# Kernel tuning notes

Hardware: AMD Instinct MI355X
Metric: run time of the kernel (lower is better)

## Reference

```python
import jax, jax.numpy as jnp
import numpy as np

NPIX = 1024
NCHAN = 4
NVIS = 200000
CELL_SIZE = 0.005  # arcsec
ARCSEC = np.pi / (180.0 * 3600.0)
DL = CELL_SIZE * ARCSEC          # radians of sky per pixel
J = 6                            # KB kernel width (torchkbnufft numpoints default)
OSF = 2                          # grid oversampling (torchkbnufft default)
G = OSF * NPIX                   # oversampled grid size
BETA = 2.34 * J                  # KB shape parameter (kbwidth*numpoints)
UV_MAX_KLAMBDA = 8000.0


def _i0(x):
    # Abramowitz & Stegun 9.8.1/9.8.2 polynomial approximation of I0(x)
    ax = jnp.abs(x)
    ts = (ax / 3.75) ** 2
    small = 1.0 + ts * (3.5156229 + ts * (3.0899424 + ts * (1.2067492
            + ts * (0.2659732 + ts * (0.0360768 + ts * 0.0045813)))))
    t = 3.75 / jnp.maximum(ax, 3.75)
    big = (jnp.exp(ax) / jnp.sqrt(jnp.maximum(ax, 3.75))) * (0.39894228
          + t * (0.01328592 + t * (0.00225319 + t * (-0.00157565
          + t * (0.00916281 + t * (-0.02057706 + t * (0.02635537
          + t * (-0.01647633 + t * 0.00392377))))))))
    return jnp.where(ax <= 3.75, small, big)


def _kb_weights(dist):
    # Kaiser-Bessel interpolation kernel, support |u| <= J/2
    s = 1.0 - (2.0 * dist / J) ** 2
    w = _i0(BETA * jnp.sqrt(jnp.maximum(s, 0.0))) / J
    return jnp.where(s > 0.0, w, 0.0)


def _apodization():
    # 1 / (continuous FT of the KB kernel) sampled at centered image coords
    n = (jnp.arange(NPIX) - NPIX // 2).astype(jnp.float32) / G
    arg = BETA ** 2 - (np.pi * J * n) ** 2
    sq = jnp.sqrt(jnp.abs(arg))
    ft = jnp.where(arg > 0, jnp.sinh(sq) / sq, jnp.sinc(sq / np.pi))
    return 1.0 / ft  # [NPIX]


def _nufft(img, uu, vv):
    # --- apodize (de-apodization pre-compensation) and zero-pad ---
    apod = _apodization()
    c = img.astype(jnp.complex64) * (apod[:, None] * apod[None, :])
    grid = jnp.zeros((NCHAN, G, G), dtype=jnp.complex64)
    grid = grid.at[:, :NPIX, :NPIX].set(c)
    # center image on grid origin so phase center = image center
    grid = jnp.roll(grid, (-(NPIX // 2), -(NPIX // 2)), axis=(1, 2))
    F = jnp.fft.fft2(grid)  # [nchan, G, G] oversampled k-space

    # --- klambda -> radians/pixel -> fractional oversampled-grid index ---
    # radpix = klambda*1e3*2pi*DL ; t = radpix * G / (2pi)
    tx = uu * (1e3 * DL * G)
    ty = vv * (1e3 * DL * G)

    # --- KB interpolation over JxJ neighborhoods ---
    offs = (jnp.arange(J) - (J // 2 - 1)).astype(jnp.float32)
    iy_f = jnp.floor(ty)[:, None] + offs[None, :]   # [nvis, J]
    ix_f = jnp.floor(tx)[:, None] + offs[None, :]
    wy = _kb_weights(ty[:, None] - iy_f)            # [nvis, J]
    wx = _kb_weights(tx[:, None] - ix_f)
    iy = jnp.mod(iy_f.astype(jnp.int32), G)
    ix = jnp.mod(ix_f.astype(jnp.int32), G)

    patch = F[:, iy[:, :, None], ix[:, None, :]]    # [nchan, nvis, J, J]
    w2 = (wy[:, :, None] * wx[:, None, :]).astype(jnp.complex64)
    return jnp.einsum('ckab,kab->ck', patch, w2)    # [nchan, nvis]


def setup_inputs() -> dict:
    key = jax.random.key(0)
    k1, k2, k3 = jax.random.split(key, 3)
    img = jax.random.normal(k1, (NCHAN, NPIX, NPIX), dtype=jnp.float32)
    uu = (jax.random.uniform(k2, (NVIS,), dtype=jnp.float32) * 2.0 - 1.0) * UV_MAX_KLAMBDA
    vv = (jax.random.uniform(k3, (NVIS,), dtype=jnp.float32) * 2.0 - 1.0) * UV_MAX_KLAMBDA
    return {"img": img, "uu": uu, "vv": vv}


def reference(img, uu, vv):
    return _nufft(img, uu, vv)
```

## Files before the change

### kernel.cpp

```cpp
#include <hip/hip_runtime.h>
#include <hip/hip_fp16.h>
#include <math.h>

#define NPIXD 1024
#define GD    2048
#define NCHAND 4
#define NVISD 200000
#define KXROWS 408
#define YPACK  832
#define FINP   1024
#define IDX(i) ((i) + ((i) >> 4))
#define RSQ2   0.70710678118654752f

#define FH_SCALE   1048576.0f
#define FH_ISCALE  (1.0f / 1048576.0f)

static constexpr double PI_D = 3.14159265358979323846;
static constexpr float SCALE_F = (float)(1000.0 * 0.005 * PI_D / (180.0 * 3600.0) * 2048.0);
static constexpr float BETA_F  = (float)(2.34 * 6.0);

__global__ void setup_kernel(float* __restrict__ apod) {
    int i = blockIdx.x * 256 + threadIdx.x;
    if (i < NPIXD) {
        float n  = (float)(i - NPIXD / 2) / (float)GD;
        float t  = (float)(PI_D * 6.0) * n;
        float arg = BETA_F * BETA_F - t * t;
        float sq  = sqrtf(fabsf(arg));
        float ft  = (arg > 0.0f) ? (sinhf(sq) / sq)
                                 : ((sq == 0.0f) ? 1.0f : (sinf(sq) / sq));
        apod[i] = 1.0f / ft;
    }
}

__device__ __forceinline__ float2 cadd(float2 a, float2 b){ return make_float2(a.x+b.x, a.y+b.y); }
__device__ __forceinline__ float2 csub(float2 a, float2 b){ return make_float2(a.x-b.x, a.y-b.y); }
__device__ __forceinline__ float2 cmulf(float2 a, float2 b){ return make_float2(a.x*b.x - a.y*b.y, a.x*b.y + a.y*b.x); }
__device__ __forceinline__ float2 cnegi(float2 a){ return make_float2(a.y, -a.x); }

__device__ __forceinline__ float2 twf(float e) {
    float s, c;
    __sincosf(e * (float)(-PI_D / 1024.0), &s, &c);
    return make_float2(c, s);
}

__device__ __forceinline__ void dft8_sparse(float2 x0, float2 x1, float2 x6, float2 x7,
                                            float2 y[8]) {
    float2 u0 = cadd(x0,x6), u1 = csub(x0,x6), u2 = cadd(x1,x7), u3 = cnegi(csub(x1,x7));
    y[0]=cadd(u0,u2); y[2]=cadd(u1,u3); y[4]=csub(u0,u2); y[6]=csub(u1,u3);
    float2 o0 = x0;
    float2 o1 = make_float2(RSQ2*(x1.x + x1.y), RSQ2*(x1.y - x1.x));
    float2 o2 = make_float2(-x6.y, x6.x);
    float2 o3 = make_float2(RSQ2*(x7.x - x7.y), RSQ2*(x7.y + x7.x));
    float2 v0 = cadd(o0,o2), v1 = csub(o0,o2), v2 = cadd(o1,o3), v3 = cnegi(csub(o1,o3));
    y[1]=cadd(v0,v2); y[3]=cadd(v1,v3); y[5]=csub(v0,v2); y[7]=csub(v1,v3);
}

__device__ __forceinline__ void dft8_full(const float2 x[8], float2 y[8]) {
    float2 e0=cadd(x[0],x[4]), e1=cadd(x[1],x[5]), e2=cadd(x[2],x[6]), e3=cadd(x[3],x[7]);
    float2 o0=csub(x[0],x[4]), o1=csub(x[1],x[5]), o2=csub(x[2],x[6]), o3=csub(x[3],x[7]);
    o1 = make_float2(RSQ2*(o1.x + o1.y), RSQ2*(o1.y - o1.x));
    o2 = cnegi(o2);
    o3 = make_float2(RSQ2*(o3.y - o3.x), -RSQ2*(o3.x + o3.y));
    float2 u0=cadd(e0,e2), u1=csub(e0,e2), u2=cadd(e1,e3), u3=cnegi(csub(e1,e3));
    y[0]=cadd(u0,u2); y[2]=cadd(u1,u3); y[4]=csub(u0,u2); y[6]=csub(u1,u3);
    float2 v0=cadd(o0,o2), v1=csub(o0,o2), v2=cadd(o1,o3), v3=cnegi(csub(o1,o3));
    y[1]=cadd(v0,v2); y[3]=cadd(v1,v3); y[5]=csub(v0,v2); y[7]=csub(v1,v3);
}

__device__ __forceinline__ void stage0_ip(float2 x0, float2 x1, float2 x6, float2 x7,
                                          float2* __restrict__ buf) {
    int j = (int)threadIdx.x;
    float2 y[8];
    dft8_sparse(x0, x1, x6, x7, y);
    buf[IDX(8 * j)] = y[0];
    #pragma unroll
    for (int t = 1; t < 8; ++t)
        buf[IDX(8 * j + t)] = cmulf(twf((float)(t * j)), y[t]);
}

__device__ __forceinline__ void r8_ip(float2* __restrict__ buf, int m) {
    int j = (int)threadIdx.x;
    float2 x[8];
    #pragma unroll
    for (int k = 0; k < 8; ++k) x[k] = buf[IDX(j + 256 * k)];
    __syncthreads();
    float2 y[8];
    dft8_full(x, y);
    int pm = j & ~(m - 1);
    int base = 7 * pm + j;
    buf[IDX(base)] = y[0];
    #pragma unroll
    for (int t = 1; t < 8; ++t)
        buf[IDX(base + t * m)] = cmulf(twf((float)(t * pm)), y[t]);
}

__device__ __forceinline__ void r4_final_ip(float2* __restrict__ buf) {
    int j = (int)threadIdx.x;
    float2 v[8];
    #pragma unroll
    for (int h = 0; h < 2; ++h) {
        int jj = j + h * 256;
        v[h*4+0] = buf[IDX(jj)];
        v[h*4+1] = buf[IDX(jj + 512)];
        v[h*4+2] = buf[IDX(jj + 1024)];
        v[h*4+3] = buf[IDX(jj + 1536)];
    }
    __syncthreads();
    #pragma unroll
    for (int h = 0; h < 2; ++h) {
        int jj = j + h * 256;
        float2 a = v[h*4], b = v[h*4+1], cc = v[h*4+2], d = v[h*4+3];
        float2 u0 = cadd(a,cc), u1 = csub(a,cc), u2 = cadd(b,d), u3 = cnegi(csub(b,d));
        buf[IDX(jj)]        = cadd(u0,u2);
        buf[IDX(jj + 1536)] = csub(u1,u3);
    }
}

__global__ __launch_bounds__(256) void fft_rows_fused(const float* __restrict__ img,
                                                      const float* __restrict__ apod,
                                                      float2* __restrict__ Fin) {
    __shared__ float2 buf[2176];
    __shared__ float2 stg[KXROWS * 9];
    int j  = (int)threadIdx.x;
    int bx = (int)blockIdx.x;
    int c  = (int)blockIdx.y;
    int w  = (bx & 7) * 16 + (bx >> 3);
    int y0 = w * 4;
    float a0 = apod[j + 512], a1 = apod[j + 768], a6 = apod[j], a7 = apod[j + 256];
    float p1[4], p2[4];
    {
        const float* r1 = img + ((size_t)c * NPIXD + y0) * NPIXD;
        const float* r2 = img + ((size_t)c * NPIXD + y0 + 512) * NPIXD;
        p1[0]=r1[j+512]; p1[1]=r1[j+768]; p1[2]=r1[j]; p1[3]=r1[j+256];
        p2[0]=r2[j+512]; p2[1]=r2[j+768]; p2[2]=r2[j]; p2[3]=r2[j+256];
    }
    #pragma unroll
    for (int p = 0; p < 4; ++p) {
        int y1 = y0 + p;
        float ay1 = apod[y1], ay2 = apod[y1 + 512];
        float2 x0 = make_float2(p1[0]*a0*ay1, p2[0]*a0*ay2);
        float2 x1 = make_float2(p1[1]*a1*ay1, p2[1]*a1*ay2);
        float2 x6 = make_float2(p1[2]*a6*ay1, p2[2]*a6*ay2);
        float2 x7 = make_float2(p1[3]*a7*ay1, p2[3]*a7*ay2);
        if (p < 3) {
            const float* q1 = img + ((size_t)c * NPIXD + y1 + 1) * NPIXD;
            const float* q2 = img + ((size_t)c * NPIXD + y1 + 513) * NPIXD;
            p1[0]=q1[j+512]; p1[1]=q1[j+768]; p1[2]=q1[j]; p1[3]=q1[j+256];
            p2[0]=q2[j+512]; p2[1]=q2[j+768]; p2[2]=q2[j]; p2[3]=q2[j+256];
        }
        __syncthreads();
        stage0_ip(x0, x1, x6, x7, buf);
        __syncthreads();
        r8_ip(buf, 8);
        __syncthreads();
        r8_ip(buf, 64);
        __syncthreads();
        r4_final_ip(buf);
        __syncthreads();
        #pragma unroll
        for (int t = 0; t < 2; ++t) {
            int kx = j + t * 256;
            if (kx < KXROWS) {
                float2 Z  = buf[IDX(kx)];
                float2 Zm = buf[IDX((GD - kx) & (GD - 1))];
                stg[kx * 9 + p]     = make_float2(0.5f*(Z.x+Zm.x), 0.5f*(Z.y-Zm.y));
                stg[kx * 9 + 4 + p] = make_float2(0.5f*(Z.y+Zm.y), 0.5f*(Zm.x-Z.x));
            }
        }
    }
    __syncthreads();
    #pragma unroll
    for (int k = 0; k < 4; ++k) {
        int m = j + 256 * k;
        if (m < 2 * KXROWS) {
            int kx = m >> 1, h = m & 1;
            float2* dst = Fin + ((size_t)c * KXROWS + kx) * FINP + y0 + h * 512;
            const float2* s = &stg[kx * 9 + h * 4];
            dst[0] = s[0]; dst[1] = s[1]; dst[2] = s[2]; dst[3] = s[3];
        }
    }
}

__global__ __launch_bounds__(256) void fft_cols(const float2* __restrict__ Fin,
                                                __half* __restrict__ FhH,
                                                float* __restrict__ FhIm,
                                                int writeIm) {
    __shared__ float2 buf[2176];
    int j = (int)threadIdx.x;
    int kx = blockIdx.x, c = blockIdx.y;
    const float2* inr = Fin + ((size_t)c * KXROWS + kx) * FINP;
    float2 x0 = inr[j + 512];
    float2 x1 = inr[j + 768];
    float2 x6 = inr[j];
    float2 x7 = inr[j + 256];
    stage0_ip(x0, x1, x6, x7, buf);
    __syncthreads();
    r8_ip(buf, 8);
    __syncthreads();
    r8_ip(buf, 64);
    __syncthreads();
    r4_final_ip(buf);
    __syncthreads();
    __half* basep = FhH + ((size_t)kx * YPACK) * NCHAND + c;
    float*  imb   = FhIm + ((size_t)c * KXROWS + kx) * YPACK;
    for (int n = j; n < GD; n += 256) {
        int pos = -1;
        if (n < 416)         pos = n + 416;
        else if (n >= 1632)  pos = n - 1632;
        if (pos >= 0) {
            float2 z = buf[IDX(n)];
            basep[(size_t)pos * NCHAND] = __float2half_rn(z.x * FH_SCALE);
            if (writeIm) imb[pos] = z.y;
        }
    }
}

__device__ __forceinline__ float i0f(float x) {
    float ax = fabsf(x);
    if (ax <= 3.75f) {
        float ts = ax / 3.75f; ts *= ts;
        return 1.0f + ts * (3.5156229f + ts * (3.0899424f + ts * (1.2067492f +
                     ts * (0.2659732f + ts * (0.0360768f + ts * 0.0045813f)))));
    } else {
        float t = 3.75f / ax;
        return expf(ax) / sqrtf(ax) *
               (0.39894228f + t * (0.01328592f + t * (0.00225319f + t * (-0.00157565f +
                t * (0.00916281f + t * (-0.02057706f + t * (0.02635537f +
                t * (-0.01647633f + t * 0.00392377f))))))));
    }
}

__device__ __forceinline__ float kbwf(float dist) {
    float r = dist * (2.0f / 6.0f);
    float s = 1.0f - r * r;
    if (s <= 0.0f) return 0.0f;
    return i0f(BETA_F * sqrtf(s)) * (1.0f / 6.0f);
}

__global__ __launch_bounds__(256) void gather6(const float* __restrict__ uu,
                                               const float* __restrict__ vv,
                                               const float4* __restrict__ FhH4,
                                               const float* __restrict__ FhIm,
                                               float* __restrict__ out,
                                               int out_elems, int complexOut) {
    int tid = (int)threadIdx.x;
    int v = tid >> 1, r = tid & 1;
    int gv = blockIdx.x * 128 + v;
    if (gv >= NVISD) return;
    float tx = uu[gv] * SCALE_F;
    float ty = vv[gv] * SCALE_F;
    float fxf = floorf(tx), fyf = floorf(ty);
    int fxi = (int)fxf, fyi = (int)fyf;

    float wx[3]; int kxr[3]; int cjr[3];
    #pragma unroll
    for (int bb = 0; bb < 3; ++bb) {
        int b = r * 3 + bb, o = b - 2;
        wx[bb] = kbwf(tx - fxf - (float)o);
        int ix = (fxi + o) & (GD - 1);
        int cj = (ix > 1024) ? 1 : 0;
        int kx = cj ? (GD - ix) : ix;
        kxr[bb] = min(kx, KXROWS - 1);
        cjr[bb] = cj;
    }
    float wy[6];
    #pragma unroll
    for (int t = 0; t < 6; ++t) wy[t] = kbwf(ty - fyf - (float)(t - 2));

    int p0n = fyi + 414, p0c = 413 - fyi;
    p0n = min(max(p0n, 0), YPACK - 6);
    p0c = min(max(p0c, 0), YPACK - 6);
    int dn = p0n & 1, dc = p0c & 1;
    int f0n = (p0n - dn) >> 1, f0c = (p0c - dc) >> 1;
    float wn8[8], wc8[8];
    #pragma unroll
    for (int w = 0; w < 8; ++w) {
        int tn = w - dn; wn8[w] = (tn >= 0 && tn < 6) ? wy[tn] : 0.0f;
        int tc = w - dc; wc8[w] = (tc >= 0 && tc < 6) ? wy[5 - tc] : 0.0f;
    }

    float s0 = 0.0f, s1 = 0.0f, s2 = 0.0f, s3 = 0.0f;
    #pragma unroll
    for (int bb = 0; bb < 3; ++bb) {
        const float4* rp = FhH4 + (size_t)kxr[bb] * (YPACK / 2);
        bool cj = cjr[bb] != 0;
        int f0 = cj ? f0c : f0n;
        float wxb = wx[bb];
        #pragma unroll
        for (int q = 0; q < 4; ++q) {
            float4 Q = rp[f0 + q];
            float w0 = wxb * (cj ? wc8[2 * q]     : wn8[2 * q]);
            float w1 = wxb * (cj ? wc8[2 * q + 1] : wn8[2 * q + 1]);
            float2 fa = __half22float2(*reinterpret_cast<const __half2*>(&Q.x));
            float2 fb = __half22float2(*reinterpret_cast<const __half2*>(&Q.y));
            float2 fc = __half22float2(*reinterpret_cast<const __half2*>(&Q.z));
            float2 fd = __half22float2(*reinterpret_cast<const __half2*>(&Q.w));
            s0 = fmaf(w0, fa.x, fmaf(w1, fc.x, s0));
            s1 = fmaf(w0, fa.y, fmaf(w1, fc.y, s1));
            s2 = fmaf(w0, fb.x, fmaf(w1, fd.x, s2));
            s3 = fmaf(w0, fb.y, fmaf(w1, fd.y, s3));
        }
    }
    s0 += __shfl_xor(s0, 1);
    s1 += __shfl_xor(s1, 1);
    s2 += __shfl_xor(s2, 1);
    s3 += __shfl_xor(s3, 1);

    if (!complexOut) {
        if (r == 0 && (size_t)3 * NVISD + gv < (size_t)out_elems) {
            out[0 * NVISD + gv] = s0 * FH_ISCALE;
            out[1 * NVISD + gv] = s1 * FH_ISCALE;
            out[2 * NVISD + gv] = s2 * FH_ISCALE;
            out[3 * NVISD + gv] = s3 * FH_ISCALE;
        }
    } else {
        float sr[4] = {s0, s1, s2, s3};
        #pragma unroll
        for (int c = 0; c < NCHAND; ++c) {
            float sy = 0.0f;
            const float* baseI = FhIm + (size_t)c * KXROWS * YPACK;
            #pragma unroll
            for (int bb = 0; bb < 3; ++bb) {
                const float* rp = baseI + (size_t)kxr[bb] * YPACK;
                bool cj = cjr[bb] != 0;
                float wxb = wx[bb];
                #pragma unroll
                for (int a = 0; a < 6; ++a) {
                    int yv = fyi + (a - 2);
                    int pos = cj ? (416 - yv) : (yv + 416);
                    pos = min(max(pos, 0), YPACK - 1);
                    float w = wxb * wy[a];
                    sy = fmaf(cj ? -w : w, rp[pos], sy);
                }
            }
            sy += __shfl_xor(sy, 1);
            size_t oidx = (size_t)c * NVISD + gv;
            if (r == 0 && 2 * oidx + 1 < (size_t)out_elems) {
                out[2 * oidx] = sr[c] * FH_ISCALE;
                out[2 * oidx + 1] = sy;
            }
        }
    }
}

extern "C" void kernel_launch(void* const* d_in, const int* in_sizes, int n_in,
                              void* d_out, int out_size, void* d_ws, size_t ws_size,
                              hipStream_t stream) {
    (void)in_sizes; (void)n_in;
    const float* img = (const float*)d_in[0];
    const float* uu  = (const float*)d_in[1];
    const float* vv  = (const float*)d_in[2];

    const size_t apodBytes = 4096;
    const size_t finBytes  = (size_t)NCHAND * KXROWS * FINP * sizeof(float2);
    const size_t fhhBytes  = (size_t)KXROWS * YPACK * NCHAND * sizeof(__half);
    const size_t fhimBytes = (size_t)NCHAND * KXROWS * YPACK * sizeof(float);
    const size_t need = apodBytes + finBytes + fhhBytes + fhimBytes;

    char* ws = (char*)d_ws;
    float*  apod = (float*)ws;
    float2* Fin  = (float2*)(ws + apodBytes);
    __half* FhH  = (__half*)(ws + apodBytes + finBytes);
    float*  FhIm = (float*)(ws + apodBytes + finBytes + fhhBytes);

    if (ws_size < need) return;

    int complexOut = (out_size >= 2 * NCHAND * NVISD) ? 1 : 0;

    setup_kernel<<<dim3(4), dim3(256), 0, stream>>>(apod);
    fft_rows_fused<<<dim3(128, NCHAND), dim3(256), 0, stream>>>(img, apod, Fin);
    fft_cols<<<dim3(KXROWS, NCHAND), dim3(256), 0, stream>>>(Fin, FhH, FhIm, complexOut);
    gather6<<<dim3((NVISD + 127) / 128), dim3(256), 0, stream>>>(
        uu, vv, (const float4*)FhH, FhIm, (float*)d_out, out_size, complexOut);
}
```

Measured before the change: 54.96 us.

## Store row-FFT intermediate as fp16, inline apodization, ping-pong buffers, widen gather split

The intermediate row-FFT output is now stored as scaled half2 instead of float2, halving the traffic between the row and column FFT kernels. The apodization setup kernel is removed and its values are computed inline with __expf, which saves one launch. The row FFT uses two shared-memory ping-pong buffers, so one barrier per stage is dropped. The gather now uses four threads per visibility instead of two. The main risk is precision loss from fp16 storage of the intermediate, and the larger shared-memory footprint may reduce occupancy.

```diff
diff --git a/kernel.cpp b/kernel.cpp
--- a/kernel.cpp
+++ b/kernel.cpp
@@ -14,22 +14,21 @@
 
 #define FH_SCALE   1048576.0f
 #define FH_ISCALE  (1.0f / 1048576.0f)
+#define FIN_SCALE  4194304.0f
+#define FIN_TO_FH  0.25f
+#define FIN_TO_IM  (1.0f / 4194304.0f)
 
 static constexpr double PI_D = 3.14159265358979323846;
 static constexpr float SCALE_F = (float)(1000.0 * 0.005 * PI_D / (180.0 * 3600.0) * 2048.0);
 static constexpr float BETA_F  = (float)(2.34 * 6.0);
 
-__global__ void setup_kernel(float* __restrict__ apod) {
-    int i = blockIdx.x * 256 + threadIdx.x;
-    if (i < NPIXD) {
-        float n  = (float)(i - NPIXD / 2) / (float)GD;
-        float t  = (float)(PI_D * 6.0) * n;
-        float arg = BETA_F * BETA_F - t * t;
-        float sq  = sqrtf(fabsf(arg));
-        float ft  = (arg > 0.0f) ? (sinhf(sq) / sq)
-                                 : ((sq == 0.0f) ? 1.0f : (sinf(sq) / sq));
-        apod[i] = 1.0f / ft;
-    }
+__device__ __forceinline__ float apodf(int i) {
+    float n  = (float)(i - 512) * (1.0f / 2048.0f);
+    float t  = (float)(PI_D * 6.0) * n;
+    float arg = BETA_F * BETA_F - t * t;
+    float sq = sqrtf(arg);
+    float e  = __expf(sq);
+    return sq * 2.0f / (e - 1.0f / e);
 }
 
 __device__ __forceinline__ float2 cadd(float2 a, float2 b){ return make_float2(a.x+b.x, a.y+b.y); }
@@ -67,15 +66,43 @@
     y[1]=cadd(v0,v2); y[3]=cadd(v1,v3); y[5]=csub(v0,v2); y[7]=csub(v1,v3);
 }
 
-__device__ __forceinline__ void stage0_ip(float2 x0, float2 x1, float2 x6, float2 x7,
-                                          float2* __restrict__ buf) {
+__device__ __forceinline__ void stage0_st(float2 x0, float2 x1, float2 x6, float2 x7,
+                                          float2* __restrict__ dst) {
     int j = (int)threadIdx.x;
     float2 y[8];
     dft8_sparse(x0, x1, x6, x7, y);
-    buf[IDX(8 * j)] = y[0];
+    dst[IDX(8 * j)] = y[0];
     #pragma unroll
     for (int t = 1; t < 8; ++t)
-        buf[IDX(8 * j + t)] = cmulf(twf((float)(t * j)), y[t]);
+        dst[IDX(8 * j + t)] = cmulf(twf((float)(t * j)), y[t]);
+}
+
+__device__ __forceinline__ void r8_st(const float2* __restrict__ src, float2* __restrict__ dst,
+                                      int m) {
+    int j = (int)threadIdx.x;
+    float2 x[8], y[8];
+    #pragma unroll
+    for (int k = 0; k < 8; ++k) x[k] = src[IDX(j + 256 * k)];
+    dft8_full(x, y);
+    int pm = j & ~(m - 1);
+    int base = 7 * pm + j;
+    dst[IDX(base)] = y[0];
+    #pragma unroll
+    for (int t = 1; t < 8; ++t)
+        dst[IDX(base + t * m)] = cmulf(twf((float)(t * pm)), y[t]);
+}
+
+__device__ __forceinline__ void r4_final_st(const float2* __restrict__ src,
+                                            float2* __restrict__ dst) {
+    #pragma unroll
+    for (int h = 0; h < 2; ++h) {
+        int jj = (int)threadIdx.x + h * 256;
+        float2 a = src[IDX(jj)], b = src[IDX(jj + 512)];
+        float2 cc = src[IDX(jj + 1024)], d = src[IDX(jj + 1536)];
+        float2 u0 = cadd(a,cc), u1 = csub(a,cc), u2 = cadd(b,d), u3 = cnegi(csub(b,d));
+        dst[IDX(jj)]        = cadd(u0,u2);
+        dst[IDX(jj + 1536)] = csub(u1,u3);
+    }
 }
 
 __device__ __forceinline__ void r8_ip(float2* __restrict__ buf, int m) {
@@ -117,16 +144,19 @@
 }
 
 __global__ __launch_bounds__(256) void fft_rows_fused(const float* __restrict__ img,
-                                                      const float* __restrict__ apod,
-                                                      float2* __restrict__ Fin) {
-    __shared__ float2 buf[2176];
-    __shared__ float2 stg[KXROWS * 9];
+                                                      unsigned int* __restrict__ FinU) {
+    __shared__ float2 bufA[2176];
+    __shared__ float2 bufB[2176];
+    __shared__ unsigned int stg[KXROWS * 9];
     int j  = (int)threadIdx.x;
     int bx = (int)blockIdx.x;
     int c  = (int)blockIdx.y;
     int w  = (bx & 7) * 16 + (bx >> 3);
     int y0 = w * 4;
-    float a0 = apod[j + 512], a1 = apod[j + 768], a6 = apod[j], a7 = apod[j + 256];
+    float a0 = apodf(j + 512), a1 = apodf(j + 768), a6 = apodf(j), a7 = apodf(j + 256);
+    float ay[8];
+    #pragma unroll
+    for (int p = 0; p < 4; ++p) { ay[p] = apodf(y0 + p); ay[4 + p] = apodf(y0 + 512 + p); }
     float p1[4], p2[4];
     {
         const float* r1 = img + ((size_t)c * NPIXD + y0) * NPIXD;
@@ -136,35 +166,35 @@
     }
     #pragma unroll
     for (int p = 0; p < 4; ++p) {
-        int y1 = y0 + p;
-        float ay1 = apod[y1], ay2 = apod[y1 + 512];
+        float ay1 = ay[p], ay2 = ay[4 + p];
         float2 x0 = make_float2(p1[0]*a0*ay1, p2[0]*a0*ay2);
         float2 x1 = make_float2(p1[1]*a1*ay1, p2[1]*a1*ay2);
         float2 x6 = make_float2(p1[2]*a6*ay1, p2[2]*a6*ay2);
         float2 x7 = make_float2(p1[3]*a7*ay1, p2[3]*a7*ay2);
         if (p < 3) {
-            const float* q1 = img + ((size_t)c * NPIXD + y1 + 1) * NPIXD;
-            const float* q2 = img + ((size_t)c * NPIXD + y1 + 513) * NPIXD;
+            const float* q1 = img + ((size_t)c * NPIXD + y0 + p + 1) * NPIXD;
+            const float* q2 = img + ((size_t)c * NPIXD + y0 + p + 513) * NPIXD;
             p1[0]=q1[j+512]; p1[1]=q1[j+768]; p1[2]=q1[j]; p1[3]=q1[j+256];
             p2[0]=q2[j+512]; p2[1]=q2[j+768]; p2[2]=q2[j]; p2[3]=q2[j+256];
         }
+        stage0_st(x0, x1, x6, x7, bufA);
         __syncthreads();
-        stage0_ip(x0, x1, x6, x7, buf);
+        r8_st(bufA, bufB, 8);
         __syncthreads();
-        r8_ip(buf, 8);
+        r8_st(bufB, bufA, 64);
         __syncthreads();
-        r8_ip(buf, 64);
-        __syncthreads();
-        r4_final_ip(buf);
+        r4_final_st(bufA, bufB);
         __syncthreads();
         #pragma unroll
         for (int t = 0; t < 2; ++t) {
             int kx = j + t * 256;
             if (kx < KXROWS) {
-                float2 Z  = buf[IDX(kx)];
-                float2 Zm = buf[IDX((GD - kx) & (GD - 1))];
-                stg[kx * 9 + p]     = make_float2(0.5f*(Z.x+Zm.x), 0.5f*(Z.y-Zm.y));
-                stg[kx * 9 + 4 + p] = make_float2(0.5f*(Z.y+Zm.y), 0.5f*(Zm.x-Z.x));
+                float2 Z  = bufB[IDX(kx)];
+                float2 Zm = bufB[IDX((GD - kx) & (GD - 1))];
+                __half2 h1 = __floats2half2_rn(0.5f*(Z.x+Zm.x)*FIN_SCALE, 0.5f*(Z.y-Zm.y)*FIN_SCALE);
+                __half2 h2 = __floats2half2_rn(0.5f*(Z.y+Zm.y)*FIN_SCALE, 0.5f*(Zm.x-Z.x)*FIN_SCALE);
+                stg[kx * 9 + p]     = *reinterpret_cast<unsigned int*>(&h1);
+                stg[kx * 9 + 4 + p] = *reinterpret_cast<unsigned int*>(&h2);
             }
         }
     }
@@ -174,26 +204,27 @@
         int m = j + 256 * k;
         if (m < 2 * KXROWS) {
             int kx = m >> 1, h = m & 1;
-            float2* dst = Fin + ((size_t)c * KXROWS + kx) * FINP + y0 + h * 512;
-            const float2* s = &stg[kx * 9 + h * 4];
-            dst[0] = s[0]; dst[1] = s[1]; dst[2] = s[2]; dst[3] = s[3];
-        }
-    }
-}
-
-__global__ __launch_bounds__(256) void fft_cols(const float2* __restrict__ Fin,
+            unsigned int* dst = FinU + ((size_t)c * KXROWS + kx) * FINP + y0 + h * 512;
+            const unsigned int* s = &stg[kx * 9 + h * 4];
+            *reinterpret_cast<uint4*>(dst) = make_uint4(s[0], s[1], s[2], s[3]);
+        }
+    }
+}
+
+__global__ __launch_bounds__(256) void fft_cols(const unsigned int* __restrict__ FinU,
                                                 __half* __restrict__ FhH,
                                                 float* __restrict__ FhIm,
                                                 int writeIm) {
     __shared__ float2 buf[2176];
     int j = (int)threadIdx.x;
     int kx = blockIdx.x, c = blockIdx.y;
-    const float2* inr = Fin + ((size_t)c * KXROWS + kx) * FINP;
-    float2 x0 = inr[j + 512];
-    float2 x1 = inr[j + 768];
-    float2 x6 = inr[j];
-    float2 x7 = inr[j + 256];
-    stage0_ip(x0, x1, x6, x7, buf);
+    const unsigned int* inr = FinU + ((size_t)c * KXROWS + kx) * FINP;
+    unsigned int u0 = inr[j + 512], u1 = inr[j + 768], u6 = inr[j], u7 = inr[j + 256];
+    float2 x0 = __half22float2(*reinterpret_cast<__half2*>(&u0));
+    float2 x1 = __half22float2(*reinterpret_cast<__half2*>(&u1));
+    float2 x6 = __half22float2(*reinterpret_cast<__half2*>(&u6));
+    float2 x7 = __half22float2(*reinterpret_cast<__half2*>(&u7));
+    stage0_st(x0, x1, x6, x7, buf);
     __syncthreads();
     r8_ip(buf, 8);
     __syncthreads();
@@ -209,8 +240,8 @@
         else if (n >= 1632)  pos = n - 1632;
         if (pos >= 0) {
             float2 z = buf[IDX(n)];
-            basep[(size_t)pos * NCHAND] = __float2half_rn(z.x * FH_SCALE);
-            if (writeIm) imb[pos] = z.y;
+            basep[(size_t)pos * NCHAND] = __float2half_rn(z.x * FIN_TO_FH);
+            if (writeIm) imb[pos] = z.y * FIN_TO_IM;
         }
     }
 }
@@ -237,15 +268,15 @@
     return i0f(BETA_F * sqrtf(s)) * (1.0f / 6.0f);
 }
 
-__global__ __launch_bounds__(256) void gather6(const float* __restrict__ uu,
+__global__ __launch_bounds__(256) void gather7(const float* __restrict__ uu,
                                                const float* __restrict__ vv,
                                                const float4* __restrict__ FhH4,
                                                const float* __restrict__ FhIm,
                                                float* __restrict__ out,
                                                int out_elems, int complexOut) {
     int tid = (int)threadIdx.x;
-    int v = tid >> 1, r = tid & 1;
-    int gv = blockIdx.x * 128 + v;
+    int v = tid >> 2, r = tid & 3;
+    int gv = blockIdx.x * 64 + v;
     if (gv >= NVISD) return;
     float tx = uu[gv] * SCALE_F;
     float ty = vv[gv] * SCALE_F;
@@ -255,7 +286,8 @@
     float wx[3]; int kxr[3]; int cjr[3];
     #pragma unroll
     for (int bb = 0; bb < 3; ++bb) {
-        int b = r * 3 + bb, o = b - 2;
+        int b = (r >> 1) * 3 + bb;
+        int o = b - 2;
         wx[bb] = kbwf(tx - fxf - (float)o);
         int ix = (fxi + o) & (GD - 1);
         int cj = (ix > 1024) ? 1 : 0;
@@ -279,6 +311,7 @@
         int tc = w - dc; wc8[w] = (tc >= 0 && tc < 6) ? wy[5 - tc] : 0.0f;
     }
 
+    int q0 = (r & 1) * 2;
     float s0 = 0.0f, s1 = 0.0f, s2 = 0.0f, s3 = 0.0f;
     #pragma unroll
     for (int bb = 0; bb < 3; ++bb) {
@@ -287,7 +320,8 @@
         int f0 = cj ? f0c : f0n;
         float wxb = wx[bb];
         #pragma unroll
-        for (int q = 0; q < 4; ++q) {
+        for (int qq = 0; qq < 2; ++qq) {
+            int q = q0 + qq;
             float4 Q = rp[f0 + q];
             float w0 = wxb * (cj ? wc8[2 * q]     : wn8[2 * q]);
             float w1 = wxb * (cj ? wc8[2 * q + 1] : wn8[2 * q + 1]);
@@ -301,10 +335,10 @@
             s3 = fmaf(w0, fb.y, fmaf(w1, fd.y, s3));
         }
     }
-    s0 += __shfl_xor(s0, 1);
-    s1 += __shfl_xor(s1, 1);
-    s2 += __shfl_xor(s2, 1);
-    s3 += __shfl_xor(s3, 1);
+    s0 += __shfl_xor(s0, 1); s0 += __shfl_xor(s0, 2);
+    s1 += __shfl_xor(s1, 1); s1 += __shfl_xor(s1, 2);
+    s2 += __shfl_xor(s2, 1); s2 += __shfl_xor(s2, 2);
+    s3 += __shfl_xor(s3, 1); s3 += __shfl_xor(s3, 2);
 
     if (!complexOut) {
         if (r == 0 && (size_t)3 * NVISD + gv < (size_t)out_elems) {
@@ -319,21 +353,24 @@
         for (int c = 0; c < NCHAND; ++c) {
             float sy = 0.0f;
             const float* baseI = FhIm + (size_t)c * KXROWS * YPACK;
-            #pragma unroll
-            for (int bb = 0; bb < 3; ++bb) {
-                const float* rp = baseI + (size_t)kxr[bb] * YPACK;
-                bool cj = cjr[bb] != 0;
-                float wxb = wx[bb];
+            if (r < 2) {
                 #pragma unroll
-                for (int a = 0; a < 6; ++a) {
-                    int yv = fyi + (a - 2);
-                    int pos = cj ? (416 - yv) : (yv + 416);
-                    pos = min(max(pos, 0), YPACK - 1);
-                    float w = wxb * wy[a];
-                    sy = fmaf(cj ? -w : w, rp[pos], sy);
+                for (int bb = 0; bb < 3; ++bb) {
+                    const float* rp = baseI + (size_t)kxr[bb] * YPACK;
+                    bool cj = cjr[bb] != 0;
+                    float wxb = wx[bb];
+                    #pragma unroll
+                    for (int a = 0; a < 6; ++a) {
+                        int yv = fyi + (a - 2);
+                        int pos = cj ? (416 - yv) : (yv + 416);
+                        pos = min(max(pos, 0), YPACK - 1);
+                        float w = wxb * wy[a];
+                        sy = fmaf(cj ? -w : w, rp[pos], sy);
+                    }
                 }
             }
-            sy += __shfl_xor(sy, 1);
+            sy = (r == 0 || r == 2) ? sy : 0.0f;
+            sy += __shfl_xor(sy, 1); sy += __shfl_xor(sy, 2);
             size_t oidx = (size_t)c * NVISD + gv;
             if (r == 0 && 2 * oidx + 1 < (size_t)out_elems) {
                 out[2 * oidx] = sr[c] * FH_ISCALE;
@@ -351,25 +388,22 @@
     const float* uu  = (const float*)d_in[1];
     const float* vv  = (const float*)d_in[2];
 
-    const size_t apodBytes = 4096;
-    const size_t finBytes  = (size_t)NCHAND * KXROWS * FINP * sizeof(float2);
+    const size_t finBytes  = (size_t)NCHAND * KXROWS * FINP * sizeof(unsigned int);
     const size_t fhhBytes  = (size_t)KXROWS * YPACK * NCHAND * sizeof(__half);
     const size_t fhimBytes = (size_t)NCHAND * KXROWS * YPACK * sizeof(float);
-    const size_t need = apodBytes + finBytes + fhhBytes + fhimBytes;
+    const size_t need = finBytes + fhhBytes + fhimBytes;
 
     char* ws = (char*)d_ws;
-    float*  apod = (float*)ws;
-    float2* Fin  = (float2*)(ws + apodBytes);
-    __half* FhH  = (__half*)(ws + apodBytes + finBytes);
-    float*  FhIm = (float*)(ws + apodBytes + finBytes + fhhBytes);
+    unsigned int* FinU = (unsigned int*)ws;
+    __half* FhH  = (__half*)(ws + finBytes);
+    float*  FhIm = (float*)(ws + finBytes + fhhBytes);
 
     if (ws_size < need) return;
 
     int complexOut = (out_size >= 2 * NCHAND * NVISD) ? 1 : 0;
 
-    setup_kernel<<<dim3(4), dim3(256), 0, stream>>>(apod);
-    fft_rows_fused<<<dim3(128, NCHAND), dim3(256), 0, stream>>>(img, apod, Fin);
-    fft_cols<<<dim3(KXROWS, NCHAND), dim3(256), 0, stream>>>(Fin, FhH, FhIm, complexOut);
-    gather6<<<dim3((NVISD + 127) / 128), dim3(256), 0, stream>>>(
+    fft_rows_fused<<<dim3(128, NCHAND), dim3(256), 0, stream>>>(img, FinU);
+    fft_cols<<<dim3(KXROWS, NCHAND), dim3(256), 0, stream>>>(FinU, FhH, FhIm, complexOut);
+    gather7<<<dim3((NVISD + 63) / 64), dim3(256), 0, stream>>>(
         uu, vv, (const float4*)FhH, FhIm, (float*)d_out, out_size, complexOut);
 }
```

New measurement: 61.38 us. 1.12x slower.
